# Optimization experiments

Measured on AMD Instinct MI355X. Metric: run time of the kernel, lower is better.

## Reference

```python
import jax, jax.numpy as jnp
import numpy as np

N_UNITS, IN, HID, BATCH = 512, 64, 64, 512
STD = float(np.sqrt(1.0 / HID))


def setup_inputs() -> dict:
    key = jax.random.key(0)
    ks = jax.random.split(key, 16)
    d = {
        "x": jax.random.normal(ks[0], (BATCH, N_UNITS, IN), jnp.float32),
        "h": jax.random.normal(ks[1], (BATCH, N_UNITS, HID), jnp.float32),
    }
    names = ["ir", "hr", "iz", "hz", "in", "hn"]
    for i, nm in enumerate(names):
        din = IN if nm.startswith("i") else HID
        d[f"W_{nm}"] = jax.random.normal(ks[2 + 2 * i], (N_UNITS, din, HID), jnp.float32) * STD
        d[f"b_{nm}"] = jax.random.normal(ks[3 + 2 * i], (N_UNITS, HID), jnp.float32) * STD
    return d


def _uwl(x, W, b):
    # per-unit linear: (B,U,din) @ (U,din,dout) + (U,dout) -> (B,U,dout)
    return jnp.einsum("bui,uio->buo", x, W) + b


def reference(x, h, W_ir, b_ir, W_hr, b_hr, W_iz, b_iz, W_hz, b_hz, W_in, b_in, W_hn, b_hn):
    r = jax.nn.sigmoid(_uwl(x, W_ir, b_ir) + _uwl(h, W_hr, b_hr))
    z = jax.nn.sigmoid(_uwl(x, W_iz, b_iz) + _uwl(h, W_hz, b_hz))
    n = jnp.tanh(_uwl(x, W_in, b_in) + r * _uwl(h, W_hn, b_hn))
    return (1.0 - z) * n + z * h
```

## Files before the change

kernel.cpp:

```cpp
#include <hip/hip_runtime.h>
#include <cstddef>

#define BATCH 512
#define UNITS 512
#define HID   64

typedef __bf16 bf16x8 __attribute__((ext_vector_type(8)));
typedef float  f32x4  __attribute__((ext_vector_type(4)));

__device__ __forceinline__ float fast_sigmoid(float v) {
    return 1.0f / (1.0f + __expf(-v));
}
__device__ __forceinline__ float fast_tanh(float v) {
    return 2.0f / (1.0f + __expf(-2.0f * v)) - 1.0f;
}

__global__ __launch_bounds__(512, 3)
void gru_kernel(const float* __restrict__ x,    const float* __restrict__ h,
                const float* __restrict__ W_ir, const float* __restrict__ b_ir,
                const float* __restrict__ W_hr, const float* __restrict__ b_hr,
                const float* __restrict__ W_iz, const float* __restrict__ b_iz,
                const float* __restrict__ W_hz, const float* __restrict__ b_hz,
                const float* __restrict__ W_in, const float* __restrict__ b_in,
                const float* __restrict__ W_hn, const float* __restrict__ b_hn,
                float* __restrict__ out)
{
    __shared__ __align__(16) unsigned char wlds[6 * 512 * 16];
    __shared__ float blds[4][64];

    const int u    = blockIdx.x;
    const int tid  = threadIdx.x;
    const int lane = tid & 63;
    const int w    = tid >> 6;
    const int lr   = lane & 15;
    const int lg   = lane >> 4;

    const float* Wg[6] = {
        W_ir + (size_t)u * 64 * 64, W_hr + (size_t)u * 64 * 64,
        W_iz + (size_t)u * 64 * 64, W_hz + (size_t)u * 64 * 64,
        W_in + (size_t)u * 64 * 64, W_hn + (size_t)u * 64 * 64 };

    {
      const int ks_s = tid >> 8;
      const int n_s  = (tid >> 6) & 3;
      const int lg_s = (tid >> 4) & 3;
      const int lr_s = tid & 15;
      const int i0   = ks_s * 32 + lg_s * 8;
      const int o_s  = n_s * 16 + lr_s;
      #pragma unroll
      for (int g = 0; g < 6; ++g) {
        const float* q = Wg[g] + (size_t)i0 * 64 + o_s;
        bf16x8 f;
        #pragma unroll
        for (int e = 0; e < 8; ++e) f[e] = (__bf16)q[(size_t)e * 64];
        *(bf16x8*)(wlds + (size_t)(g * 512 + tid) * 16) = f;
      }
    }

    if (tid < 256) {
      const int o_l = tid & 63;
      const int which = tid >> 6;
      const int o = u * 64 + o_l;
      float v;
      if      (which == 0) v = b_ir[o] + b_hr[o];
      else if (which == 1) v = b_iz[o] + b_hz[o];
      else if (which == 2) v = b_in[o];
      else                 v = b_hn[o];
      blds[which][o_l] = v;
    }

    __syncthreads();

    const f32x4 zero4 = { 0.0f, 0.0f, 0.0f, 0.0f };
    const int loff = lane * 16;

    #pragma unroll 1
    for (int it = 0; it < 4; ++it) {
      const int brow0 = it * 128 + w * 16;

      bf16x8 ax[2], ah[2];
      {
        const int row = brow0 + lr;
        const float* px = x + ((size_t)row * UNITS + u) * HID;
        const float* ph = h + ((size_t)row * UNITS + u) * HID;
        #pragma unroll
        for (int ks = 0; ks < 2; ++ks) {
          const int i0 = ks * 32 + lg * 8;
          f32x4 xv0 = *(const f32x4*)(px + i0);
          f32x4 xv1 = *(const f32x4*)(px + i0 + 4);
          f32x4 hv0 = *(const f32x4*)(ph + i0);
          f32x4 hv1 = *(const f32x4*)(ph + i0 + 4);
          bf16x8 fx, fh;
          #pragma unroll
          for (int e = 0; e < 4; ++e) {
            fx[e]     = (__bf16)xv0[e];
            fx[4 + e] = (__bf16)xv1[e];
            fh[e]     = (__bf16)hv0[e];
            fh[4 + e] = (__bf16)hv1[e];
          }
          ax[ks] = fx;
          ah[ks] = fh;
        }
      }

      #pragma unroll 1
      for (int n = 0; n < 4; ++n) {
        const int o = n * 16 + lr;

        float hv[4];
        #pragma unroll
        for (int j = 0; j < 4; ++j) {
          const int row = brow0 + lg * 4 + j;
          hv[j] = h[((size_t)row * UNITS + u) * HID + o];
        }
        const float br = blds[0][o];
        const float bz = blds[1][o];
        const float bi = blds[2][o];
        const float bh = blds[3][o];

        f32x4 accr = zero4, accz = zero4, acca = zero4, accb = zero4;
        #pragma unroll
        for (int ks = 0; ks < 2; ++ks) {
          const unsigned char* bp = wlds + ks * 4096 + n * 1024 + loff;
          bf16x8 b0 = *(const bf16x8*)(bp + 0 * 8192);
          bf16x8 b1 = *(const bf16x8*)(bp + 1 * 8192);
          bf16x8 b2 = *(const bf16x8*)(bp + 2 * 8192);
          bf16x8 b3 = *(const bf16x8*)(bp + 3 * 8192);
          bf16x8 b4 = *(const bf16x8*)(bp + 4 * 8192);
          bf16x8 b5 = *(const bf16x8*)(bp + 5 * 8192);
          accr = __builtin_amdgcn_mfma_f32_16x16x32_bf16(ax[ks], b0, accr, 0, 0, 0);
          accr = __builtin_amdgcn_mfma_f32_16x16x32_bf16(ah[ks], b1, accr, 0, 0, 0);
          accz = __builtin_amdgcn_mfma_f32_16x16x32_bf16(ax[ks], b2, accz, 0, 0, 0);
          accz = __builtin_amdgcn_mfma_f32_16x16x32_bf16(ah[ks], b3, accz, 0, 0, 0);
          acca = __builtin_amdgcn_mfma_f32_16x16x32_bf16(ax[ks], b4, acca, 0, 0, 0);
          accb = __builtin_amdgcn_mfma_f32_16x16x32_bf16(ah[ks], b5, accb, 0, 0, 0);
        }

        #pragma unroll
        for (int j = 0; j < 4; ++j) {
          const int row = brow0 + lg * 4 + j;
          const size_t idx = ((size_t)row * UNITS + u) * HID + o;
          const float rv = fast_sigmoid(accr[j] + br);
          const float zv = fast_sigmoid(accz[j] + bz);
          const float nv = fast_tanh(acca[j] + bi + rv * (accb[j] + bh));
          out[idx] = (1.0f - zv) * nv + zv * hv[j];
        }
      }
    }
}

extern "C" void kernel_launch(void* const* d_in, const int* in_sizes, int n_in,
                              void* d_out, int out_size, void* d_ws, size_t ws_size,
                              hipStream_t stream) {
    const float* x    = (const float*)d_in[0];
    const float* h    = (const float*)d_in[1];
    const float* W_ir = (const float*)d_in[2];
    const float* b_ir = (const float*)d_in[3];
    const float* W_hr = (const float*)d_in[4];
    const float* b_hr = (const float*)d_in[5];
    const float* W_iz = (const float*)d_in[6];
    const float* b_iz = (const float*)d_in[7];
    const float* W_hz = (const float*)d_in[8];
    const float* b_hz = (const float*)d_in[9];
    const float* W_in = (const float*)d_in[10];
    const float* b_in = (const float*)d_in[11];
    const float* W_hn = (const float*)d_in[12];
    const float* b_hn = (const float*)d_in[13];
    float* out = (float*)d_out;

    gru_kernel<<<dim3(UNITS), dim3(512), 0, stream>>>(
        x, h, W_ir, b_ir, W_hr, b_hr, W_iz, b_iz, W_hz, b_hz,
        W_in, b_in, W_hn, b_hn, out);
}
```

Before: 55.60 us.

## Prefetch next x/h tile into registers and use hardware reciprocal in activations

Issues global loads for the first x/h tile before the weight staging into LDS, and inside the batch loop prefetches the next iteration's x/h rows into registers while the MFMA and epilogue work of the current tile runs. Sigmoid and tanh now use the hardware reciprocal instead of a full-precision divide. Launch bounds are lowered from 3 to 2 blocks per SM to give the extra live prefetch registers room, which may reduce occupancy.

Measured after the change: 55.54 us. About the same (-0.1%).

```diff
diff --git a/kernel.cpp b/kernel.cpp
--- a/kernel.cpp
+++ b/kernel.cpp
@@ -9,13 +9,13 @@
 typedef float  f32x4  __attribute__((ext_vector_type(4)));
 
 __device__ __forceinline__ float fast_sigmoid(float v) {
-    return 1.0f / (1.0f + __expf(-v));
+    return __builtin_amdgcn_rcpf(1.0f + __expf(-v));
 }
 __device__ __forceinline__ float fast_tanh(float v) {
-    return 2.0f / (1.0f + __expf(-2.0f * v)) - 1.0f;
+    return 2.0f * __builtin_amdgcn_rcpf(1.0f + __expf(-2.0f * v)) - 1.0f;
 }
 
-__global__ __launch_bounds__(512, 3)
+__global__ __launch_bounds__(512, 2)
 void gru_kernel(const float* __restrict__ x,    const float* __restrict__ h,
                 const float* __restrict__ W_ir, const float* __restrict__ b_ir,
                 const float* __restrict__ W_hr, const float* __restrict__ b_hr,
@@ -34,6 +34,24 @@
     const int w    = tid >> 6;
     const int lr   = lane & 15;
     const int lg   = lane >> 4;
+
+    const float* pxB = x + ((size_t)(w * 16 + lr) * UNITS + u) * HID;
+    const float* phB = h + ((size_t)(w * 16 + lr) * UNITS + u) * HID;
+    const size_t istep = (size_t)128 * UNITS * HID;
+
+    f32x4 rx0, rx1, rx2, rx3, rh0, rh1, rh2, rh3;
+    {
+      const int k0 = lg * 8;
+      const int k1 = 32 + lg * 8;
+      rx0 = *(const f32x4*)(pxB + k0);
+      rx1 = *(const f32x4*)(pxB + k0 + 4);
+      rx2 = *(const f32x4*)(pxB + k1);
+      rx3 = *(const f32x4*)(pxB + k1 + 4);
+      rh0 = *(const f32x4*)(phB + k0);
+      rh1 = *(const f32x4*)(phB + k0 + 4);
+      rh2 = *(const f32x4*)(phB + k1);
+      rh3 = *(const f32x4*)(phB + k1 + 4);
+    }
 
     const float* Wg[6] = {
         W_ir + (size_t)u * 64 * 64, W_hr + (size_t)u * 64 * 64,
@@ -80,27 +98,34 @@
 
       bf16x8 ax[2], ah[2];
       {
-        const int row = brow0 + lr;
-        const float* px = x + ((size_t)row * UNITS + u) * HID;
-        const float* ph = h + ((size_t)row * UNITS + u) * HID;
+        bf16x8 f;
         #pragma unroll
-        for (int ks = 0; ks < 2; ++ks) {
-          const int i0 = ks * 32 + lg * 8;
-          f32x4 xv0 = *(const f32x4*)(px + i0);
-          f32x4 xv1 = *(const f32x4*)(px + i0 + 4);
-          f32x4 hv0 = *(const f32x4*)(ph + i0);
-          f32x4 hv1 = *(const f32x4*)(ph + i0 + 4);
-          bf16x8 fx, fh;
-          #pragma unroll
-          for (int e = 0; e < 4; ++e) {
-            fx[e]     = (__bf16)xv0[e];
-            fx[4 + e] = (__bf16)xv1[e];
-            fh[e]     = (__bf16)hv0[e];
-            fh[4 + e] = (__bf16)hv1[e];
-          }
-          ax[ks] = fx;
-          ah[ks] = fh;
-        }
+        for (int e = 0; e < 4; ++e) { f[e] = (__bf16)rx0[e]; f[4+e] = (__bf16)rx1[e]; }
+        ax[0] = f;
+        #pragma unroll
+        for (int e = 0; e < 4; ++e) { f[e] = (__bf16)rx2[e]; f[4+e] = (__bf16)rx3[e]; }
+        ax[1] = f;
+        #pragma unroll
+        for (int e = 0; e < 4; ++e) { f[e] = (__bf16)rh0[e]; f[4+e] = (__bf16)rh1[e]; }
+        ah[0] = f;
+        #pragma unroll
+        for (int e = 0; e < 4; ++e) { f[e] = (__bf16)rh2[e]; f[4+e] = (__bf16)rh3[e]; }
+        ah[1] = f;
+      }
+
+      if (it < 3) {
+        const float* px = pxB + (size_t)(it + 1) * istep;
+        const float* ph = phB + (size_t)(it + 1) * istep;
+        const int k0 = lg * 8;
+        const int k1 = 32 + lg * 8;
+        rx0 = *(const f32x4*)(px + k0);
+        rx1 = *(const f32x4*)(px + k0 + 4);
+        rx2 = *(const f32x4*)(px + k1);
+        rx3 = *(const f32x4*)(px + k1 + 4);
+        rh0 = *(const f32x4*)(ph + k0);
+        rh1 = *(const f32x4*)(ph + k0 + 4);
+        rh2 = *(const f32x4*)(ph + k1);
+        rh3 = *(const f32x4*)(ph + k1 + 4);
       }
 
       #pragma unroll 1
```
